# Kernel optimization log

Measured on AMD Instinct MI355X. Metric: run time of the kernel, lower is better.

## Reference

```python
import jax, jax.numpy as jnp
import numpy as np

INPUT_SIZE = 4096
HIDDEN = 1024
WINDOW = 2048
STRIDE = 1024
METRIC = 32
POOLING = "last"


def setup_inputs() -> dict:
    key = jax.random.key(0)
    ks = jax.random.split(key, 9)
    s = 1.0 / np.sqrt(HIDDEN)  # torch LSTMCell/Linear init bound
    u = lambda k, shape: jax.random.uniform(k, shape, jnp.float32, -s, s)
    return {
        "inp": jax.random.normal(ks[0], (WINDOW, INPUT_SIZE), jnp.float32),
        "h1": jax.random.normal(ks[1], (1, HIDDEN), jnp.float32),
        "c1": jax.random.normal(ks[2], (1, HIDDEN), jnp.float32),
        "W_ih": u(ks[3], (4 * HIDDEN, INPUT_SIZE)),
        "W_hh": u(ks[4], (4 * HIDDEN, HIDDEN)),
        "b_ih": u(ks[5], (4 * HIDDEN,)),
        "b_hh": u(ks[6], (4 * HIDDEN,)),
        "fc_w": u(ks[7], (METRIC, HIDDEN)),
        "fc_b": u(ks[8], (METRIC,)),
    }


def reference(inp, h1, c1, W_ih, W_hh, b_ih, b_hh, fc_w, fc_b):
    window = min(WINDOW, inp.shape[0])
    # Precompute the input-side gate projection as one GEMM: [T, 4H]
    xg = inp[:window] @ W_ih.T + b_ih

    def step(carry, xg_t):
        h, c = carry  # each [1, H]
        gates = xg_t + h @ W_hh.T + b_hh  # [1, 4H]
        i, f, g, o = jnp.split(gates, 4, axis=-1)
        c = jax.nn.sigmoid(f) * c + jax.nn.sigmoid(i) * jnp.tanh(g)
        h = jax.nn.sigmoid(o) * jnp.tanh(c)
        return (h, c), (h, c)

    (h_fin, c_fin), (hs, cs) = jax.lax.scan(step, (h1, c1), xg)

    if window >= STRIDE:
        h_last = jax.lax.stop_gradient(hs[STRIDE - 1])  # [1, H], detached
        c_last = jax.lax.stop_gradient(cs[STRIDE - 1])
    else:
        h_last, c_last = None, None

    if POOLING == "mean":
        # mean of fc(h_i) over last STRIDE steps of the window
        out = (hs[window - STRIDE:, 0, :] @ fc_w.T + fc_b).sum(axis=0, keepdims=True) / STRIDE
    else:  # 'last'
        out = h_fin @ fc_w.T + fc_b  # [1, METRIC]
    out = jnp.tanh(out)
    return out, h_last, c_last
```

## Files before the change

kernel.cpp:

```cpp
#include <hip/hip_runtime.h>
#include <stdint.h>

typedef unsigned short u16;
typedef unsigned long long u64;
typedef __attribute__((ext_vector_type(8))) short short8;
typedef __attribute__((ext_vector_type(4))) float floatx4;

#define K_IN    4096
#define HID     1024
#define G4H     4096
#define T_STEPS 2048
#define NWG     128
#define SPIN_MAX 60000

__device__ __forceinline__ u16 f2bf(float f) {
  union { float f; unsigned int i; } v; v.f = f;
  unsigned int lsb = (v.i >> 16) & 1u;
  v.i += 0x7fffu + lsb;
  return (u16)(v.i >> 16);
}
__device__ __forceinline__ float finz(float x) {
  unsigned b = __float_as_uint(x);
  return ((b & 0x7f800000u) == 0x7f800000u) ? 0.f : x;
}
__device__ __forceinline__ float sigm(float x) {
  x = fminf(30.f, fmaxf(-30.f, finz(x)));
  return 1.0f / (1.0f + __expf(-x));
}
__device__ __forceinline__ float tanh_s(float x) {
  x = fminf(15.f, fmaxf(-15.f, finz(x)));
  float e = __expf(2.0f * x);
  return (e - 1.0f) / (e + 1.0f);
}

__device__ __forceinline__ void publish_h(u64* hx, int slot, int idx, float h) {
  h = finz(h);
  u64 v = ((u64)(unsigned)(slot + 1) << 32) | (u64)__float_as_uint(h);
  __hip_atomic_store(&hx[(size_t)slot * HID + idx], v,
                     __ATOMIC_RELAXED, __HIP_MEMORY_SCOPE_AGENT);
}

__device__ __forceinline__ void poll2(const u64* hx, int slot, int j0,
                                      float* v, int* alive) {
  const u64* p = hx + (size_t)slot * HID + j0;
  const unsigned tag = (unsigned)(slot + 1);
  if (*alive) {
    int spins = 0;
    for (;;) {
      u64 a = __hip_atomic_load(&p[0], __ATOMIC_RELAXED, __HIP_MEMORY_SCOPE_AGENT);
      u64 b = __hip_atomic_load(&p[1], __ATOMIC_RELAXED, __HIP_MEMORY_SCOPE_AGENT);
      if ((unsigned)(a >> 32) == tag && (unsigned)(b >> 32) == tag) {
        v[0] = finz(__uint_as_float((unsigned)a));
        v[1] = finz(__uint_as_float((unsigned)b));
        return;
      }
      if (++spins > SPIN_MAX) { *alive = 0; break; }
      __builtin_amdgcn_s_sleep(1);
    }
  }
  v[0] = v[1] = 0.f;
}

__global__ __launch_bounds__(256) void cvt_bf16_k(const float* __restrict__ src,
                                                  u16* __restrict__ dst, int n4) {
  int i = blockIdx.x * 256 + threadIdx.x;
  if (i < n4) {
    float4 v = *(const float4*)(src + (size_t)i * 4);
    u16 o0 = f2bf(v.x), o1 = f2bf(v.y), o2 = f2bf(v.z), o3 = f2bf(v.w);
    ushort4 o = {o0, o1, o2, o3};
    *(ushort4*)(dst + (size_t)i * 4) = o;
  }
}

__global__ __launch_bounds__(256) void xg_gemm_k(const u16* __restrict__ A,
                                                 const u16* __restrict__ B,
                                                 const float* __restrict__ bias,
                                                 float* __restrict__ C)
{
  __shared__ __align__(16) u16 As[128 * 64];
  __shared__ __align__(16) u16 Bs[128 * 64];
  const int tid  = threadIdx.x;
  const int lane = tid & 63;
  const int quad = lane >> 4;
  const int l16  = lane & 15;
  const int wid  = tid >> 6;
  const int wm   = wid >> 1, wn = wid & 1;
  const int tileM = blockIdx.y * 128;
  const int tileN = blockIdx.x * 128;

  floatx4 acc[4][4];
  #pragma unroll
  for (int mi = 0; mi < 4; ++mi)
    #pragma unroll
    for (int ni = 0; ni < 4; ++ni)
      acc[mi][ni] = (floatx4){0.f, 0.f, 0.f, 0.f};

  for (int k0 = 0; k0 < K_IN; k0 += 64) {
    #pragma unroll
    for (int i = 0; i < 4; ++i) {
      int c = i * 256 + tid;
      int row = c >> 3, col = (c & 7) * 8;
      *(short8*)(As + c * 8) = *(const short8*)(A + (size_t)(tileM + row) * K_IN + k0 + col);
      *(short8*)(Bs + c * 8) = *(const short8*)(B + (size_t)(tileN + row) * K_IN + k0 + col);
    }
    __syncthreads();
    #pragma unroll
    for (int kk = 0; kk < 64; kk += 32) {
      short8 av[4], bv[4];
      #pragma unroll
      for (int mi = 0; mi < 4; ++mi)
        av[mi] = *(const short8*)(As + (wm * 64 + mi * 16 + l16) * 64 + kk + quad * 8);
      #pragma unroll
      for (int ni = 0; ni < 4; ++ni)
        bv[ni] = *(const short8*)(Bs + (wn * 64 + ni * 16 + l16) * 64 + kk + quad * 8);
      #pragma unroll
      for (int mi = 0; mi < 4; ++mi)
        #pragma unroll
        for (int ni = 0; ni < 4; ++ni)
          acc[mi][ni] = __builtin_amdgcn_mfma_f32_16x16x32_bf16(av[mi], bv[ni], acc[mi][ni], 0, 0, 0);
    }
    __syncthreads();
  }
  #pragma unroll
  for (int ni = 0; ni < 4; ++ni) {
    int n = tileN + wn * 64 + ni * 16 + l16;
    float bn = bias[n];
    #pragma unroll
    for (int mi = 0; mi < 4; ++mi) {
      int mbase = tileM + wm * 64 + mi * 16 + quad * 4;
      #pragma unroll
      for (int r = 0; r < 4; ++r)
        C[(size_t)(mbase + r) * G4H + n] = acc[mi][ni][r] + bn;
    }
  }
}

__global__ __launch_bounds__(512, 1) void lstm_scan_k(const float* __restrict__ Whh,
                                                      const float* __restrict__ bhh,
                                                      const float* __restrict__ h1,
                                                      const float* __restrict__ c1,
                                                      const float* __restrict__ fcw,
                                                      const float* __restrict__ fcb,
                                                      const float* __restrict__ xg,
                                                      u64* hx,
                                                      float* out)
{
  const int g    = blockIdx.x;
  const int tid  = threadIdx.x;
  const int lane = tid & 63;
  const int w    = tid >> 6;
  const int q    = w >> 1;
  const int ub   = (w & 1) * 4;

  __shared__ float h_local[HID];
  __shared__ float gsum[32];
  __shared__ float xgb[2][32];
  __shared__ float bhhb[32];
  __shared__ float pp[32][16];

  float wreg[4][16];
  #pragma unroll
  for (int i = 0; i < 4; ++i) {
    const size_t row = (size_t)(q * HID + g * 8 + ub + i);
    #pragma unroll
    for (int j = 0; j < 16; ++j)
      wreg[i][j] = Whh[row * HID + j * 64 + lane];
  }
  if (tid < 32) bhhb[tid] = bhh[(tid >> 3) * HID + g * 8 + (tid & 7)];

  float c_state = 0.f;
  if (tid < 8) {
    c_state = c1[g * 8 + tid];
    publish_h(hx, 0, g * 8 + tid, h1[g * 8 + tid]);
  }

  int alive = 1;
  const int j0 = tid * 2;
  for (int t = 0; t < T_STEPS; ++t) {
    float xval = 0.f;
    if (tid < 32) xval = finz(xg[(size_t)t * G4H + (tid >> 3) * HID + g * 8 + (tid & 7)]);
    float v[2];
    poll2(hx, t, j0, v, &alive);
    h_local[j0 + 0] = v[0]; h_local[j0 + 1] = v[1];
    if (tid < 32) xgb[t & 1][tid] = xval;
    __syncthreads();

    float s[4] = {0.f, 0.f, 0.f, 0.f};
    #pragma unroll
    for (int j = 0; j < 16; ++j) {
      float hv = h_local[j * 64 + lane];
      #pragma unroll
      for (int i = 0; i < 4; ++i) s[i] = fmaf(wreg[i][j], hv, s[i]);
    }
    #pragma unroll
    for (int d = 1; d < 64; d <<= 1) {
      #pragma unroll
      for (int i = 0; i < 4; ++i) s[i] += __shfl_xor(s[i], d, 64);
    }
    if (lane == 0) {
      #pragma unroll
      for (int i = 0; i < 4; ++i) gsum[q * 8 + ub + i] = s[i];
    }
    __syncthreads();

    if (tid < 8) {
      const int u = tid;
      const float* xb = xgb[t & 1];
      float gi = gsum[u]      + xb[u]      + bhhb[u];
      float gf = gsum[8 + u]  + xb[8 + u]  + bhhb[8 + u];
      float gg = gsum[16 + u] + xb[16 + u] + bhhb[16 + u];
      float go = gsum[24 + u] + xb[24 + u] + bhhb[24 + u];
      float iv = sigm(gi), fv = sigm(gf), gv = tanh_s(gg), ov = sigm(go);
      c_state = finz(fv * c_state + iv * gv);
      float hval = ov * tanh_s(c_state);
      publish_h(hx, t + 1, g * 8 + u, hval);
      if (t == 1023) {
        out[32 + g * 8 + u]       = finz(hval);
        out[32 + HID + g * 8 + u] = finz(c_state);
      }
    }
  }

  if (g == 0) {
    float v[2];
    poll2(hx, T_STEPS, j0, v, &alive);
    h_local[j0 + 0] = v[0]; h_local[j0 + 1] = v[1];
    __syncthreads();
    const int m = tid >> 4, seg = tid & 15;
    float pacc = 0.f;
    for (int k = seg * 64; k < seg * 64 + 64; ++k)
      pacc = fmaf(fcw[m * HID + k], h_local[k], pacc);
    pp[m][seg] = finz(pacc);
    __syncthreads();
    if (tid < 32) {
      float sum = fcb[tid];
      #pragma unroll
      for (int i = 0; i < 16; ++i) sum += pp[tid][i];
      out[tid] = tanh_s(finz(sum));
    }
  }
}

extern "C" void kernel_launch(void* const* d_in, const int* in_sizes, int n_in,
                              void* d_out, int out_size, void* d_ws, size_t ws_size,
                              hipStream_t stream) {
  const float* inp = (const float*)d_in[0];
  const float* h1  = (const float*)d_in[1];
  const float* c1  = (const float*)d_in[2];
  const float* Wih = (const float*)d_in[3];
  const float* Whh = (const float*)d_in[4];
  const float* bih = (const float*)d_in[5];
  const float* bhh = (const float*)d_in[6];
  const float* fcw = (const float*)d_in[7];
  const float* fcb = (const float*)d_in[8];
  float* out = (float*)d_out;

  const size_t xg_bytes  = (size_t)T_STEPS * G4H * 4;
  const size_t hx_bytes  = (size_t)(T_STEPS + 1) * HID * 8;
  const size_t ab_bytes  = (size_t)T_STEPS * K_IN * 2;
  const size_t wb_bytes  = (size_t)G4H * K_IN * 2;
  if (ws_size < xg_bytes + hx_bytes + ab_bytes + wb_bytes) return;

  float* xg   = (float*)d_ws;
  u64*   hx   = (u64*)((char*)d_ws + xg_bytes);
  u16*   Abf  = (u16*)((char*)d_ws + xg_bytes + hx_bytes);
  u16*   Wbf  = (u16*)((char*)d_ws + xg_bytes + hx_bytes + ab_bytes);

  const int nA4 = T_STEPS * K_IN / 4;
  const int nW4 = G4H * K_IN / 4;
  cvt_bf16_k<<<dim3((nA4 + 255) / 256), 256, 0, stream>>>(inp, Abf, nA4);
  cvt_bf16_k<<<dim3((nW4 + 255) / 256), 256, 0, stream>>>(Wih, Wbf, nW4);
  xg_gemm_k<<<dim3(G4H / 128, T_STEPS / 128), 256, 0, stream>>>(Abf, Wbf, bih, xg);
  lstm_scan_k<<<dim3(NWG), 512, 0, stream>>>(Whh, bhh, h1, c1, fcw, fcb, xg, hx, out);
}
```

Measured before the change: 4.807 ms.

## Give each wave one hidden unit, drop second barrier, use DPP reductions

After: 7.154 ms. 1.49x slower.

```diff
diff --git a/kernel.cpp b/kernel.cpp
--- a/kernel.cpp
+++ b/kernel.cpp
@@ -61,6 +61,11 @@
   v[0] = v[1] = 0.f;
 }
 
+__device__ __forceinline__ float bcast63(float x) {
+  int i = __builtin_amdgcn_readlane(__builtin_bit_cast(int, x), 63);
+  return __builtin_bit_cast(float, i);
+}
+
 __global__ __launch_bounds__(256) void cvt_bf16_k(const float* __restrict__ src,
                                                   u16* __restrict__ dst, int n4) {
   int i = blockIdx.x * 256 + threadIdx.x;
@@ -149,74 +154,74 @@
   const int tid  = threadIdx.x;
   const int lane = tid & 63;
   const int w    = tid >> 6;
-  const int q    = w >> 1;
-  const int ub   = (w & 1) * 4;
-
-  __shared__ float h_local[HID];
-  __shared__ float gsum[32];
-  __shared__ float xgb[2][32];
-  __shared__ float bhhb[32];
+  const int u    = g * 8 + w;
+
+  __shared__ __align__(16) float hb[2][HID];
   __shared__ float pp[32][16];
 
-  float wreg[4][16];
+  floatx4 wreg[4][4];
   #pragma unroll
   for (int i = 0; i < 4; ++i) {
-    const size_t row = (size_t)(q * HID + g * 8 + ub + i);
-    #pragma unroll
-    for (int j = 0; j < 16; ++j)
-      wreg[i][j] = Whh[row * HID + j * 64 + lane];
-  }
-  if (tid < 32) bhhb[tid] = bhh[(tid >> 3) * HID + g * 8 + (tid & 7)];
-
-  float c_state = 0.f;
-  if (tid < 8) {
-    c_state = c1[g * 8 + tid];
-    publish_h(hx, 0, g * 8 + tid, h1[g * 8 + tid]);
-  }
+    const float* wr = Whh + (size_t)(i * HID + u) * HID;
+    #pragma unroll
+    for (int j = 0; j < 4; ++j)
+      wreg[i][j] = *(const floatx4*)(wr + j * 256 + lane * 4);
+  }
+  const float bh0 = bhh[u], bh1 = bhh[HID + u], bh2 = bhh[2 * HID + u], bh3 = bhh[3 * HID + u];
+
+  float c_state = c1[u];
+  if (lane == 0) publish_h(hx, 0, u, h1[u]);
 
   int alive = 1;
   const int j0 = tid * 2;
   for (int t = 0; t < T_STEPS; ++t) {
-    float xval = 0.f;
-    if (tid < 32) xval = finz(xg[(size_t)t * G4H + (tid >> 3) * HID + g * 8 + (tid & 7)]);
+    const float* xgt = xg + (size_t)t * G4H;
+    float xv0 = xgt[u], xv1 = xgt[HID + u], xv2 = xgt[2 * HID + u], xv3 = xgt[3 * HID + u];
+
     float v[2];
     poll2(hx, t, j0, v, &alive);
-    h_local[j0 + 0] = v[0]; h_local[j0 + 1] = v[1];
-    if (tid < 32) xgb[t & 1][tid] = xval;
-    __syncthreads();
-
-    float s[4] = {0.f, 0.f, 0.f, 0.f};
-    #pragma unroll
-    for (int j = 0; j < 16; ++j) {
-      float hv = h_local[j * 64 + lane];
-      #pragma unroll
-      for (int i = 0; i < 4; ++i) s[i] = fmaf(wreg[i][j], hv, s[i]);
-    }
-    #pragma unroll
-    for (int d = 1; d < 64; d <<= 1) {
-      #pragma unroll
-      for (int i = 0; i < 4; ++i) s[i] += __shfl_xor(s[i], d, 64);
-    }
+    float* hl = hb[t & 1];
+    hl[j0 + 0] = v[0]; hl[j0 + 1] = v[1];
+    __syncthreads();
+
+    float s0 = 0.f, s1 = 0.f, s2 = 0.f, s3 = 0.f;
+    #pragma unroll
+    for (int j = 0; j < 4; ++j) {
+      floatx4 hv = *(const floatx4*)(hl + j * 256 + lane * 4);
+      #pragma unroll
+      for (int k = 0; k < 4; ++k) {
+        s0 = fmaf(wreg[0][j][k], hv[k], s0);
+        s1 = fmaf(wreg[1][j][k], hv[k], s1);
+        s2 = fmaf(wreg[2][j][k], hv[k], s2);
+        s3 = fmaf(wreg[3][j][k], hv[k], s3);
+      }
+    }
+
+#define DPP_LEVEL(mods) \
+    asm("v_add_f32 %0, %0, %0 " mods : "+v"(s0)); \
+    asm("v_add_f32 %0, %0, %0 " mods : "+v"(s1)); \
+    asm("v_add_f32 %0, %0, %0 " mods : "+v"(s2)); \
+    asm("v_add_f32 %0, %0, %0 " mods : "+v"(s3));
+    DPP_LEVEL("row_shr:1 bound_ctrl:0")
+    DPP_LEVEL("row_shr:2 bound_ctrl:0")
+    DPP_LEVEL("row_shr:4 bank_mask:0xe")
+    DPP_LEVEL("row_shr:8 bank_mask:0xc")
+    DPP_LEVEL("row_bcast:15 row_mask:0xa")
+    DPP_LEVEL("row_bcast:31 row_mask:0xc")
+#undef DPP_LEVEL
+
+    float gi = bcast63(s0) + xv0 + bh0;
+    float gf = bcast63(s1) + xv1 + bh1;
+    float gg = bcast63(s2) + xv2 + bh2;
+    float go = bcast63(s3) + xv3 + bh3;
+    float iv = sigm(gi), fv = sigm(gf), gv = tanh_s(gg), ov = sigm(go);
+    c_state = finz(fv * c_state + iv * gv);
+    float hval = ov * tanh_s(c_state);
     if (lane == 0) {
-      #pragma unroll
-      for (int i = 0; i < 4; ++i) gsum[q * 8 + ub + i] = s[i];
-    }
-    __syncthreads();
-
-    if (tid < 8) {
-      const int u = tid;
-      const float* xb = xgb[t & 1];
-      float gi = gsum[u]      + xb[u]      + bhhb[u];
-      float gf = gsum[8 + u]  + xb[8 + u]  + bhhb[8 + u];
-      float gg = gsum[16 + u] + xb[16 + u] + bhhb[16 + u];
-      float go = gsum[24 + u] + xb[24 + u] + bhhb[24 + u];
-      float iv = sigm(gi), fv = sigm(gf), gv = tanh_s(gg), ov = sigm(go);
-      c_state = finz(fv * c_state + iv * gv);
-      float hval = ov * tanh_s(c_state);
-      publish_h(hx, t + 1, g * 8 + u, hval);
+      publish_h(hx, t + 1, u, hval);
       if (t == 1023) {
-        out[32 + g * 8 + u]       = finz(hval);
-        out[32 + HID + g * 8 + u] = finz(c_state);
+        out[32 + u]       = finz(hval);
+        out[32 + HID + u] = finz(c_state);
       }
     }
   }
@@ -224,12 +229,13 @@
   if (g == 0) {
     float v[2];
     poll2(hx, T_STEPS, j0, v, &alive);
-    h_local[j0 + 0] = v[0]; h_local[j0 + 1] = v[1];
+    float* hl = hb[0];
+    hl[j0 + 0] = v[0]; hl[j0 + 1] = v[1];
     __syncthreads();
     const int m = tid >> 4, seg = tid & 15;
     float pacc = 0.f;
     for (int k = seg * 64; k < seg * 64 + 64; ++k)
-      pacc = fmaf(fcw[m * HID + k], h_local[k], pacc);
+      pacc = fmaf(fcw[m * HID + k], hl[k], pacc);
     pp[m][seg] = finz(pacc);
     __syncthreads();
     if (tid < 32) {
```
